# Kernel optimization log

Measured on AMD Instinct MI355X. Metric: run time of the kernel, lower is better.

## Reference

```python
import jax, jax.numpy as jnp
import numpy as np
import math

D = 128
RATIO = 0.8
BN_EPS = 1e-5
N_NODES = 40000
N_EDGES = 640000
Y_SIZE = 8


def _prelu(x, a):
    return jnp.where(x > 0, x, a * x)


def setup_inputs() -> dict:
    key = jax.random.key(0)
    ks = jax.random.split(key, 16)
    inv = lambda n: 1.0 / np.sqrt(n)
    return {
        "x": jax.random.normal(ks[0], (N_NODES, 1), jnp.float32),
        "edge_index": jax.random.randint(ks[1], (2, N_EDGES), 0, N_NODES, jnp.int32),
        "W1": jax.random.normal(ks[2], (1, D), jnp.float32),
        "V1": jax.random.normal(ks[3], (1, D), jnp.float32),
        "Ws": jax.random.normal(ks[4], (9, D, D), jnp.float32) * inv(D),
        "Vs": jax.random.normal(ks[5], (9, D, D), jnp.float32) * inv(D),
        "conv_b": jax.random.normal(ks[6], (10, D), jnp.float32) * 0.01,
        "bn_gamma": 1.0 + 0.1 * jax.random.normal(ks[7], (10, D), jnp.float32),
        "bn_beta": 0.1 * jax.random.normal(ks[8], (10, D), jnp.float32),
        "bn_mean": jnp.zeros((10, D), jnp.float32),
        "bn_var": jnp.ones((10, D), jnp.float32),
        "pool_p": jax.random.normal(ks[9], (10, D), jnp.float32),
        "prelu_a": 0.25 * jnp.ones((1,), jnp.float32),
        "lin1_w": jax.random.normal(ks[10], (2560, 1280), jnp.float32) * inv(2560),
        "lin1_b": jax.random.normal(ks[11], (1280,), jnp.float32) * 0.01,
        "lin2_w": jax.random.normal(ks[12], (1280, Y_SIZE), jnp.float32) * inv(1280),
        "lin2_b": jax.random.normal(ks[13], (Y_SIZE,), jnp.float32) * 0.01,
    }


def reference(x, edge_index, W1, V1, Ws, Vs, conv_b, bn_gamma, bn_beta, bn_mean,
              bn_var, pool_p, prelu_a, lin1_w, lin1_b, lin2_w, lin2_b):
    # Single graph (batch all zeros). Edge array stays fixed size with a validity mask.
    src, dst = edge_index[0], edge_index[1]
    emask = jnp.ones(src.shape, dtype=bool)
    n = x.shape[0]
    h = x
    reads = []
    for i in range(10):
        W = W1 if i == 0 else Ws[i - 1]
        V = V1 if i == 0 else Vs[i - 1]
        # ---- ARMAConv (num_stacks=1, num_layers=1): relu(L_hat (h W) + h V + b)
        ew = emask.astype(h.dtype)
        deg = jax.ops.segment_sum(ew, dst, num_segments=n)
        dinv = jnp.where(deg > 0, 1.0 / jnp.sqrt(deg), 0.0)
        norm = dinv[dst] * dinv[src] * ew                      # [E]
        hw = h @ W                                             # [n, D]
        agg = jax.ops.segment_sum(hw[src] * norm[:, None], dst, num_segments=n)
        h = jax.nn.relu(agg + h @ V + conv_b[i])
        # ---- BatchNorm1d (eval mode, running stats)
        h = (h - bn_mean[i]) * (bn_gamma[i] / jnp.sqrt(bn_var[i] + BN_EPS)) + bn_beta[i]
        # ---- shared PReLU
        h = _prelu(h, prelu_a)
        # ---- TopKPooling(ratio=0.8): score = tanh(h.p/||p||), keep ceil(0.8n)
        p = pool_p[i]
        score = jnp.tanh(h @ p / jnp.linalg.norm(p))
        k = math.ceil(RATIO * n)
        topv, idx = jax.lax.top_k(score, k)
        h = h[idx] * topv[:, None]                             # [k, D]
        remap = jnp.full((n,), -1, jnp.int32).at[idx].set(jnp.arange(k, dtype=jnp.int32))
        ns, nd = remap[src], remap[dst]
        emask = emask & (ns >= 0) & (nd >= 0)
        src = jnp.where(emask, ns, 0)
        dst = jnp.where(emask, nd, 0)
        n = k
        # ---- global max + mean pool (single graph)
        reads.append(jnp.concatenate([h.max(axis=0), h.mean(axis=0)]))
    r = jnp.concatenate(reads)[None, :]                        # [1, 2560]
    z = _prelu(r @ lin1_w + lin1_b, prelu_a)                   # dropout = identity (eval)
    z = _prelu(z @ lin2_w + lin2_b, prelu_a)
    z = z - z.min(axis=1, keepdims=True)
    z = z / z.max(axis=1, keepdims=True)
    z = z / z.sum(axis=1, keepdims=True)
    return z
```

## Files before the change

kernel.cpp:

```cpp
#include <hip/hip_runtime.h>
#include <hip/hip_bf16.h>

#define NEDGE 640000
#define NMAX  40000
#define SB    40
#define PRB   256
#define EBLK  512
#define FB    1280
#define LIN1B 64
#define GRB   8
#define HTS   12
#define TKB   32
#define GHN   5632
#define GBMAX 4096

__device__ inline unsigned orderKey(float s) {
    unsigned b = __float_as_uint(s);
    return (b & 0x80000000u) ? ~b : (b | 0x80000000u);
}

__device__ inline void histAdd(int* sh, int bin, bool act, int nbits) {
    unsigned long long mm = __ballot(act);
    for (int b = 0; b < nbits; b++) {
        unsigned long long bal = __ballot(act && ((bin >> b) & 1));
        mm &= ((bin >> b) & 1) ? bal : ~bal;
    }
    if (act) {
        int lane = threadIdx.x & 63;
        int leader = __ffsll(mm) - 1;
        if (lane == leader) atomicAdd(&sh[bin], __popcll(mm));
    }
}

__device__ inline void gridbar(int* ctr, int target) {
    __syncthreads();
    if (threadIdx.x == 0) {
        __threadfence();
        __hip_atomic_fetch_add(ctr, 1, __ATOMIC_RELEASE, __HIP_MEMORY_SCOPE_AGENT);
        while (__hip_atomic_load(ctr, __ATOMIC_ACQUIRE, __HIP_MEMORY_SCOPE_AGENT) < target)
            __builtin_amdgcn_s_sleep(1);
        __threadfence();
    }
    __syncthreads();
}

__device__ inline int waveScanIncl(int v) {
    int lane = threadIdx.x & 63;
    #pragma unroll
    for (int off = 1; off < 64; off <<= 1) {
        int o = __shfl_up(v, off);
        if (lane >= off) v += o;
    }
    return v;
}

__device__ inline void selScan2048(const int* gh, int rem, int* outD, int* outR, int* outCnt) {
    __shared__ int wtot[16];
    __shared__ int s_T;
    int t = threadIdx.x, lane = t & 63, wid = t >> 6;
    int a0 = gh[2*t], a1 = gh[2*t+1];
    int s  = a0 + a1;
    int ws = waveScanIncl(s);
    if (lane == 63) wtot[wid] = ws;
    __syncthreads();
    if (t < 16) {
        int v = wtot[t];
        #pragma unroll
        for (int off = 1; off < 16; off <<= 1) { int o = __shfl_up(v, off); if (lane >= off) v += o; }
        wtot[t] = v;
        if (t == 15) s_T = v;
    }
    __syncthreads();
    int base = (wid > 0) ? wtot[wid-1] : 0;
    int inclPair = base + ws;
    int P1 = inclPair - a1;
    int P0 = P1 - a0;
    int Q = s_T - rem;
    if (a0 > 0 && P0 <= Q && Q < P0 + a0) { *outD = 2*t;   *outR = a0 - (Q - P0); *outCnt = a0; }
    if (a1 > 0 && P1 <= Q && Q < P1 + a1) { *outD = 2*t+1; *outR = a1 - (Q - P1); *outCnt = a1; }
    __syncthreads();
}

__device__ inline void selScan1024(const int* gh, int rem, int* outD, int* outR, int* outCnt) {
    __shared__ int wtot[16];
    __shared__ int s_T;
    int t = threadIdx.x, lane = t & 63, wid = t >> 6;
    int a0 = gh[t];
    int ws = waveScanIncl(a0);
    if (lane == 63) wtot[wid] = ws;
    __syncthreads();
    if (t < 16) {
        int v = wtot[t];
        #pragma unroll
        for (int off = 1; off < 16; off <<= 1) { int o = __shfl_up(v, off); if (lane >= off) v += o; }
        wtot[t] = v;
        if (t == 15) s_T = v;
    }
    __syncthreads();
    int base = (wid > 0) ? wtot[wid-1] : 0;
    int P0 = base + ws - a0;
    int Q = s_T - rem;
    if (a0 > 0 && P0 <= Q && Q < P0 + a0) { *outD = t; *outR = a0 - (Q - P0); *outCnt = a0; }
    __syncthreads();
}

__device__ inline void prefixSel256(int* lh, const int* gh, int rem, int* outD, int* outR) {
    int t = threadIdx.x;
    if (t < 256) lh[t] = gh[t];
    __syncthreads();
    for (int off = 1; off < 256; off <<= 1) {
        int v = 0;
        if (t < 256) v = lh[t] + ((t >= off) ? lh[t-off] : 0);
        __syncthreads();
        if (t < 256) lh[t] = v;
        __syncthreads();
    }
    if (t < 256) {
        int P = lh[t], Pp = (t == 0) ? 0 : lh[t-1];
        if (P >= rem && Pp < rem) { *outD = t; *outR = rem - Pp; }
    }
    __syncthreads();
}

__device__ inline void poolReduceC(const float* __restrict__ scr, float* __restrict__ rbuf,
                                   int gbP, int L, int ch) {
    int t = threadIdx.x;
    bool isMax = ch < 128;
    float acc = isMax ? -3.402823e38f : 0.f;
    for (int r = t; r < gbP; r += 256) {
        float v = scr[(size_t)r*256 + ch];
        acc = isMax ? fmaxf(acc, v) : (acc + v);
    }
    __shared__ float red[256];
    red[t] = acc; __syncthreads();
    for (int st = 128; st > 0; st >>= 1) {
        if (t < st) red[t] = isMax ? fmaxf(red[t], red[t+st]) : (red[t] + red[t+st]);
        __syncthreads();
    }
    if (t == 0) rbuf[L*256 + ch] = red[0];
}

__device__ const float c_invk[10] = {
    1.0f/32000.0f, 1.0f/25600.0f, 1.0f/20480.0f, 1.0f/16384.0f, 1.0f/13108.0f,
    1.0f/10487.0f, 1.0f/8390.0f,  1.0f/6712.0f,  1.0f/5370.0f,  1.0f/4296.0f };

__global__ void k_init(const int* __restrict__ eidx, int* __restrict__ esrc,
                       int* __restrict__ edst, int* __restrict__ erank,
                       const float* __restrict__ poolp,
                       float* __restrict__ rbuf, float* __restrict__ pnorm,
                       int* __restrict__ ecnt, int* __restrict__ degA,
                       int* __restrict__ tkc) {
    int b = blockIdx.x, t = threadIdx.x;
    if (b < 10) {
        rbuf[b*256 + t] = (t < 128) ? -3.402823e38f : 0.0f;
        __shared__ float red[256];
        float v = 0.0f;
        if (t < 128) { float pv = poolp[b*128 + t]; v = pv*pv; }
        red[t] = v; __syncthreads();
        for (int s = 128; s > 0; s >>= 1) { if (t < s) red[t] += red[t+s]; __syncthreads(); }
        if (t == 0) pnorm[b] = sqrtf(red[0]);
    }
    if (b == 10 && t < 16) ecnt[t] = (t == 0) ? NEDGE : 0;
    if (b == 11 && t < 64) tkc[t] = 0;
    int e = b*256 + t;
    if (e < NEDGE) {
        int d = eidx[NEDGE + e];
        esrc[e] = eidx[e]; edst[e] = d;
        erank[e] = atomicAdd(&degA[d], 1);
    }
}

__global__ __launch_bounds__(256) void k_presum(const int* __restrict__ deg,
                                                int* __restrict__ lbsum,
                                                int n, int chunk) {
    int b = blockIdx.x, t = threadIdx.x;
    __shared__ int red[256];
    int start = b*chunk, end = min(start + chunk, n);
    int s = 0;
    for (int i = start + t; i < end; i += 256) s += deg[i];
    red[t] = s; __syncthreads();
    for (int st = 128; st > 0; st >>= 1) { if (t < st) red[t] += red[t+st]; __syncthreads(); }
    if (t == 0) lbsum[b] = red[0];
}

__global__ void k_scan(const int* __restrict__ deg,
                       int* __restrict__ offs, float* __restrict__ dinv,
                       int* __restrict__ ghist, int* __restrict__ selbuf,
                       const int* __restrict__ lbsum,
                       const float* __restrict__ scr, float* __restrict__ rbuf,
                       int n, int chunk, int gbP, int prevL) {
    int b = blockIdx.x, t = threadIdx.x, lane = t & 63, wid = t >> 6;
    if (b >= SB) {
        if (gbP > 0) poolReduceC(scr, rbuf, gbP, prevL, b - SB);
        return;
    }
    __shared__ int s_excl;
    __shared__ int wsum[4];
    __shared__ int s_carry;
    __shared__ int s_sums[SB];
    if (b == 0) {
        for (int jj = t; jj < GHN; jj += 256) ghist[jj] = 0;
        if (t == 0) { selbuf[2] = 0; selbuf[5] = 0; }
    }
    if (t < SB) s_sums[t] = lbsum[t];
    __syncthreads();
    if (t == 0) {
        int excl = 0;
        for (int p = 0; p < b; p++) excl += s_sums[p];
        s_excl = excl;
    }
    __syncthreads();
    if (t == 0) s_carry = s_excl;
    __syncthreads();
    int start = b*chunk, end = min(start + chunk, n);
    for (int base = start; base < end; base += 256) {
        int i = base + t;
        int d = (i < end) ? deg[i] : 0;
        int incl = d;
        for (int off = 1; off < 64; off <<= 1) {
            int o = __shfl_up(incl, off);
            if (lane >= off) incl += o;
        }
        if (lane == 63) wsum[wid] = incl;
        __syncthreads();
        if (t == 0) { int c = s_carry; for (int w = 0; w < 4; w++) { int tmp = wsum[w]; wsum[w] = c; c += tmp; } s_carry = c; }
        __syncthreads();
        int p = wsum[wid] + incl - d;
        if (i < end) {
            offs[i] = p;
            dinv[i] = (d > 0) ? 1.0f/sqrtf((float)d) : 0.0f;
        }
        __syncthreads();
    }
}

__global__ __launch_bounds__(128) void k_fill(const int* __restrict__ esrc, const int* __restrict__ edst,
                                              const int* __restrict__ erank, const int* __restrict__ offs,
                                              int* __restrict__ csr, const int* __restrict__ ecnt) {
    int ec = *ecnt;
    for (int e = blockIdx.x*128 + threadIdx.x; e < ec; e += FB*128)
        csr[offs[edst[e]] + erank[e]] = esrc[e];
}

__global__ __launch_bounds__(128) void k_gather0(
    const float* __restrict__ x, const float* __restrict__ W1, const float* __restrict__ V1,
    const float* __restrict__ convb,
    const float* __restrict__ bng, const float* __restrict__ bnb,
    const float* __restrict__ bnm, const float* __restrict__ bnv,
    const float* __restrict__ poolp, const float* __restrict__ pnorm,
    const float* __restrict__ prelua,
    const int* __restrict__ offs, const int* __restrict__ deg, const float* __restrict__ dinv,
    const int* __restrict__ csr,
    float* __restrict__ AGG, float* __restrict__ score, unsigned* __restrict__ keys) {
    int v = blockIdx.x, j = threadIdx.x;
    __shared__ float red[128];
    int off = offs[v], dg = deg[v];
    float accs = 0.0f;
    for (int c = j; c < dg; c += 128) { int s = csr[off + c]; accs += x[s]*dinv[s]; }
    red[j] = accs; __syncthreads();
    for (int st = 64; st > 0; st >>= 1) { if (j < st) red[j] += red[j+st]; __syncthreads(); }
    float aggs = red[0] * dinv[v];
    __syncthreads();
    float h2 = aggs*W1[j] + x[v]*V1[j] + convb[j];
    h2 = fmaxf(h2, 0.0f);
    float scale = bng[j] / sqrtf(bnv[j] + 1e-5f);
    h2 = (h2 - bnm[j])*scale + bnb[j];
    float a = prelua[0];
    h2 = (h2 > 0.0f) ? h2 : a*h2;
    AGG[v*128 + j] = h2;
    red[j] = h2 * poolp[j]; __syncthreads();
    for (int st = 64; st > 0; st >>= 1) { if (j < st) red[j] += red[j+st]; __syncthreads(); }
    if (j == 0) {
        float sc = tanhf(red[0] / pnorm[0]);
        score[v] = sc;
        keys[v]  = orderKey(sc);
    }
}

__global__ __launch_bounds__(128) void k_gather(
    const float* __restrict__ HW, float* __restrict__ AGG,
    const int* __restrict__ offs, const int* __restrict__ deg, const float* __restrict__ dinv,
    const int* __restrict__ csr,
    const float* __restrict__ bng, const float* __restrict__ bnb,
    const float* __restrict__ bnm, const float* __restrict__ bnv,
    const float* __restrict__ poolp, const float* __restrict__ pnorm,
    const float* __restrict__ prelua,
    float* __restrict__ score, unsigned* __restrict__ keys, int layer) {
    int v = blockIdx.x, j = threadIdx.x;
    __shared__ int   s_src[128];
    __shared__ float s_dv[128];
    __shared__ float red[128];
    int off = offs[v], dg = deg[v];
    float acc = 0.0f;
    for (int base = 0; base < dg; base += 128) {
        int cnt = min(128, dg - base);
        if (j < cnt) { int s = csr[off + base + j]; s_src[j] = s; s_dv[j] = dinv[s]; }
        __syncthreads();
        for (int c = 0; c < cnt; c++) acc += HW[s_src[c]*128 + j] * s_dv[c];
        __syncthreads();
    }
    int gj = layer*128 + j;
    float h2 = AGG[v*128 + j] + acc*dinv[v];
    h2 = fmaxf(h2, 0.0f);
    float scale = bng[gj] / sqrtf(bnv[gj] + 1e-5f);
    h2 = (h2 - bnm[gj])*scale + bnb[gj];
    float a = prelua[0];
    h2 = (h2 > 0.0f) ? h2 : a*h2;
    AGG[v*128 + j] = h2;
    red[j] = h2 * poolp[gj]; __syncthreads();
    for (int st = 64; st > 0; st >>= 1) { if (j < st) red[j] += red[j+st]; __syncthreads(); }
    if (j == 0) {
        float sc = tanhf(red[0] / pnorm[layer]);
        score[v] = sc;
        keys[v]  = orderKey(sc);
    }
}

__global__ __launch_bounds__(1024) void k_topk(const unsigned* __restrict__ keys,
                                               int* __restrict__ gh, int* __restrict__ selbuf,
                                               int* __restrict__ degN,
                                               int* __restrict__ remap, int* __restrict__ keep_ids,
                                               int* __restrict__ bar, int n, int kk) {
    __shared__ int lh[2048];
    __shared__ int s_d1, s_r1, s_c1, s_dA, s_rA, s_cA, s_dB, s_ntk, s_cnt3, s_bC, s_r2, s_lowD, s_lowR;
    __shared__ int s_base, s_cur;
    int t = threadIdx.x, b = blockIdx.x, lane = t & 63;
    int* h1 = gh;
    int* h2 = gh + 2048;
    int* h3 = gh + 4096;
    int* h4 = gh + 5120;
    int* h5 = gh + 5376;

    for (int i = b*1024 + t; i < NMAX; i += TKB*1024) degN[i] = 0;

    int nR = (n + 1023) & ~1023;
    lh[t] = 0; lh[t+1024] = 0;
    __syncthreads();
    for (int i = b*1024 + t; i < nR; i += TKB*1024) {
        bool act = (i < n);
        int bin = act ? (int)(keys[i] >> 21) : 0;
        histAdd(lh, bin, act, 11);
    }
    __syncthreads();
    { int c = lh[t]; if (c) atomicAdd(&h1[t], c); c = lh[t+1024]; if (c) atomicAdd(&h1[t+1024], c); }
    gridbar(&bar[0], TKB);
    selScan2048(h1, kk, &s_d1, &s_r1, &s_c1);
    int bstar = s_d1;

    lh[t] = 0; lh[t+1024] = 0;
    __syncthreads();
    for (int i = b*1024 + t; i < nR; i += TKB*1024) {
        bool act = false; int bin = 0;
        if (i < n) { unsigned key = keys[i]; act = ((int)(key >> 21) == bstar); bin = (int)((key >> 10) & 2047); }
        histAdd(lh, act ? bin : 0, act, 11);
    }
    __syncthreads();
    { int c = lh[t]; if (c) atomicAdd(&h2[t], c); c = lh[t+1024]; if (c) atomicAdd(&h2[t+1024], c); }
    gridbar(&bar[1], TKB);
    selScan2048(h2, s_r1, &s_dA, &s_rA, &s_cA);
    unsigned top21 = ((unsigned)bstar << 11) | (unsigned)s_dA;

    lh[t] = 0;
    __syncthreads();
    for (int i = b*1024 + t; i < nR; i += TKB*1024) {
        bool act = false; int bin = 0;
        if (i < n) { unsigned key = keys[i]; act = ((key >> 10) == top21); bin = (int)(key & 1023); }
        histAdd(lh, act ? bin : 0, act, 10);
    }
    __syncthreads();
    { int c = lh[t]; if (c) atomicAdd(&h3[t], c); }
    gridbar(&bar[2], TKB);
    selScan1024(h3, s_rA, &s_dB, &s_ntk, &s_cnt3);
    unsigned thresh = (top21 << 10) | (unsigned)s_dB;

    int cut;
    if (s_cnt3 == s_ntk) {
        cut = n - 1;
    } else {
        if (t < 256) lh[t] = 0;
        __syncthreads();
        for (int i = b*1024 + t; i < n; i += TKB*1024)
            if (keys[i] == thresh) atomicAdd(&lh[i >> 8], 1);
        __syncthreads();
        if (t < 256) { int c = lh[t]; if (c) atomicAdd(&h4[t], c); }
        gridbar(&bar[3], TKB);
        prefixSel256(lh, h4, s_ntk, &s_bC, &s_r2);
        int bC = s_bC;

        if (t < 256) lh[t] = 0;
        __syncthreads();
        for (int i = b*1024 + t; i < n; i += TKB*1024)
            if (keys[i] == thresh && (i >> 8) == bC) atomicAdd(&lh[i & 255], 1);
        __syncthreads();
        if (t < 256) { int c = lh[t]; if (c) atomicAdd(&h5[t], c); }
        gridbar(&bar[4], TKB);
        prefixSel256(lh, h5, s_r2, &s_lowD, &s_lowR);
        cut = (bC << 8) | s_lowD;
    }

    {
        int cnt = 0;
        for (int base = b*1024; base < n; base += TKB*1024) {
            int i = base + t;
            if (i < n) {
                unsigned key = keys[i];
                cnt += (key > thresh) || (key == thresh && i <= cut);
            }
        }
        lh[t] = cnt; __syncthreads();
        for (int st = 512; st > 0; st >>= 1) { if (t < st) lh[t] += lh[t+st]; __syncthreads(); }
        if (t == 0) { s_base = atomicAdd(&selbuf[5], lh[0]); s_cur = 0; }
        __syncthreads();
        for (int base = b*1024; base < n; base += TKB*1024) {
            int i = base + t;
            bool keep = false;
            if (i < n) {
                unsigned key = keys[i];
                keep = (key > thresh) || (key == thresh && i <= cut);
            }
            unsigned long long m = __ballot(keep);
            int wcnt = __popcll(m);
            int wbase = 0;
            if (lane == 0 && wcnt) wbase = atomicAdd(&s_cur, wcnt);
            wbase = __shfl(wbase, 0);
            if (keep) {
                int slot = s_base + wbase + __popcll(m & ((1ULL << lane) - 1));
                remap[i] = slot; keep_ids[slot] = i;
            } else if (i < n) remap[i] = -1;
        }
    }
}

__global__ __launch_bounds__(128) void k_poolgemm(
        const float* __restrict__ AGGc, const float* __restrict__ score,
        const int* __restrict__ keep_ids, const int* __restrict__ remap,
        float* __restrict__ scr,
        const int* __restrict__ esrcP, const int* __restrict__ edstP,
        int* __restrict__ esrcN, int* __restrict__ edstN, int* __restrict__ erankN,
        const int* __restrict__ ecntP, int* __restrict__ ecntN, int* __restrict__ degN,
        const float* __restrict__ W, const float* __restrict__ V, const float* __restrict__ bias,
        float* __restrict__ HW, float* __restrict__ AGGn, int k, int gb, int do_gemm) {
    int b = blockIdx.x, t = threadIdx.x;
    __shared__ __align__(16) float ht[128*HTS];
    if (b < gb) {
        int v0 = b * GRB;
        float mx = -3.402823e38f, sm = 0.f;
        #pragma unroll
        for (int it = 0; it < GRB; it++) {
            int r = v0 + it;
            bool valid = (r < k);
            int vv = keep_ids[valid ? r : (k - 1)];
            float val = AGGc[(size_t)vv*128 + t] * score[vv];
            if (!valid) val = 0.f;
            ht[t*HTS + it] = val;
            if (valid) { mx = fmaxf(mx, val); sm += val; }
        }
        scr[b*256 + t]       = mx;
        scr[b*256 + 128 + t] = sm;
        if (!do_gemm) return;
        __syncthreads();
        float accW[GRB], accV[GRB];
        #pragma unroll
        for (int r = 0; r < GRB; r++) { accW[r] = 0.0f; accV[r] = 0.0f; }
        #pragma unroll 4
        for (int kk = 0; kk < 128; kk++) {
            float mw = W[kk*128 + t];
            float mv = V[kk*128 + t];
            const float* hp = &ht[kk*HTS];
            #pragma unroll
            for (int r4 = 0; r4 < GRB; r4 += 4) {
                float4 hq = *(const float4*)(hp + r4);
                accW[r4+0] += hq.x*mw;  accV[r4+0] += hq.x*mv;
                accW[r4+1] += hq.y*mw;  accV[r4+1] += hq.y*mv;
                accW[r4+2] += hq.z*mw;  accV[r4+2] += hq.z*mv;
                accW[r4+3] += hq.w*mw;  accV[r4+3] += hq.w*mv;
            }
        }
        float bb = bias[t];
        #pragma unroll
        for (int r = 0; r < GRB; r++) {
            int v = v0 + r;
            if (v >= k) break;
            HW[(size_t)v*128 + t]   = accW[r];
            AGGn[(size_t)v*128 + t] = accV[r] + bb;
        }
    } else {
        int eb = b - gb, lane = t & 63;
        int ec = *ecntP;
        int* red = (int*)ht;
        __shared__ int s_base, s_cur;
        int cnt = 0;
        for (int base = eb*128; base < ec; base += EBLK*128) {
            int e = base + t;
            if (e < ec) {
                int ns = remap[esrcP[e]], nd = remap[edstP[e]];
                cnt += (ns >= 0 && nd >= 0);
            }
        }
        red[t] = cnt; __syncthreads();
        for (int st = 64; st > 0; st >>= 1) { if (t < st) red[t] += red[t+st]; __syncthreads(); }
        if (t == 0) { s_base = atomicAdd(ecntN, red[0]); s_cur = 0; }
        __syncthreads();
        for (int base = eb*128; base < ec; base += EBLK*128) {
            int e = base + t;
            bool keep = false; int ns = 0, nd = 0;
            if (e < ec) {
                ns = remap[esrcP[e]]; nd = remap[edstP[e]];
                keep = (ns >= 0 && nd >= 0);
            }
            unsigned long long m = __ballot(keep);
            int wcnt = __popcll(m);
            int wbase = 0;
            if (lane == 0 && wcnt) wbase = atomicAdd(&s_cur, wcnt);
            wbase = __shfl(wbase, 0);
            if (keep) {
                int pos = s_base + wbase + __popcll(m & ((1ULL << lane) - 1));
                esrcN[pos] = ns; edstN[pos] = nd;
                erankN[pos] = atomicAdd(&degN[nd], 1);
            }
        }
    }
}

__global__ __launch_bounds__(256) void k_pred(const float* __restrict__ scr, float* __restrict__ rbuf,
                                              int gbP, int L) {
    poolReduceC(scr, rbuf, gbP, L, blockIdx.x);
}

__global__ __launch_bounds__(320) void k_lin1(const float* __restrict__ rbuf,
                                              const float* __restrict__ w1,
                                              float* __restrict__ z1part) {
    int b = blockIdx.x, t = threadIdx.x;
    int j = t*4;
    float4 acc = make_float4(0.f, 0.f, 0.f, 0.f);
    int i0 = b*40;
    for (int r = 0; r < 40; r++) {
        int i = i0 + r;
        float rv = rbuf[i];
        if (i & 128) rv *= c_invk[i >> 8];
        float4 w = *(const float4*)(w1 + (size_t)i*1280 + j);
        acc.x += rv*w.x; acc.y += rv*w.y; acc.z += rv*w.z; acc.w += rv*w.w;
    }
    *(float4*)(z1part + b*1280 + j) = acc;
}

__global__ __launch_bounds__(320) void k_lin2(const float* __restrict__ z1part,
                                              const float* __restrict__ b1,
                                              const float* __restrict__ w2, const float* __restrict__ b2,
                                              const float* __restrict__ prelua, float* __restrict__ out) {
    int t = threadIdx.x, lane = t & 63, wid = t >> 6;
    float a = prelua[0];
    int j = t*4;
    float4 acc = make_float4(0.f, 0.f, 0.f, 0.f);
    for (int p = 0; p < LIN1B; p++) {
        float4 v = *(const float4*)(z1part + p*1280 + j);
        acc.x += v.x; acc.y += v.y; acc.z += v.z; acc.w += v.w;
    }
    float4 bb = *(const float4*)(b1 + j);
    float z0 = acc.x + bb.x; z0 = z0 > 0.f ? z0 : a*z0;
    float z1 = acc.y + bb.y; z1 = z1 > 0.f ? z1 : a*z1;
    float z2 = acc.z + bb.z; z2 = z2 > 0.f ? z2 : a*z2;
    float z3 = acc.w + bb.w; z3 = z3 > 0.f ? z3 : a*z3;
    float s[8];
    #pragma unroll
    for (int o = 0; o < 8; o++)
        s[o] = z0*w2[(j+0)*8+o] + z1*w2[(j+1)*8+o] + z2*w2[(j+2)*8+o] + z3*w2[(j+3)*8+o];
    #pragma unroll
    for (int off = 32; off > 0; off >>= 1)
        #pragma unroll
        for (int o = 0; o < 8; o++) s[o] += __shfl_down(s[o], off);
    __shared__ float sred[5][8];
    if (lane == 0)
        for (int o = 0; o < 8; o++) sred[wid][o] = s[o];
    __syncthreads();
    if (t == 0) {
        float zo[8];
        for (int o = 0; o < 8; o++) {
            float z = sred[0][o]+sred[1][o]+sred[2][o]+sred[3][o]+sred[4][o] + b2[o];
            zo[o] = z > 0.f ? z : a*z;
        }
        float mn = zo[0];
        for (int o = 1; o < 8; o++) mn = fminf(mn, zo[o]);
        float v[8], mx = -3.402823e38f;
        for (int o = 0; o < 8; o++) { v[o] = zo[o] - mn; mx = fmaxf(mx, v[o]); }
        float sm = 0.f;
        for (int o = 0; o < 8; o++) { v[o] = v[o] / mx; sm += v[o]; }
        for (int o = 0; o < 8; o++) out[o] = v[o] / sm;
    }
}

extern "C" void kernel_launch(void* const* d_in, const int* in_sizes, int n_in,
                              void* d_out, int out_size, void* d_ws, size_t ws_size,
                              hipStream_t stream) {
    const float* x      = (const float*)d_in[0];
    const int*   eidx   = (const int*)  d_in[1];
    const float* W1     = (const float*)d_in[2];
    const float* V1     = (const float*)d_in[3];
    const float* Ws     = (const float*)d_in[4];
    const float* Vs     = (const float*)d_in[5];
    const float* convb  = (const float*)d_in[6];
    const float* bng    = (const float*)d_in[7];
    const float* bnb    = (const float*)d_in[8];
    const float* bnm    = (const float*)d_in[9];
    const float* bnv    = (const float*)d_in[10];
    const float* poolp  = (const float*)d_in[11];
    const float* prelua = (const float*)d_in[12];
    const float* w1     = (const float*)d_in[13];
    const float* b1     = (const float*)d_in[14];
    const float* w2     = (const float*)d_in[15];
    const float* b2     = (const float*)d_in[16];
    float* out = (float*)d_out;

    float* wsf  = (float*)d_ws;
    float* aggA   = wsf;
    float* aggB   = aggA  + (size_t)NMAX*128;
    float* HW     = aggB  + (size_t)NMAX*128;
    float* dinv   = HW    + (size_t)NMAX*128;
    float* score  = dinv  + NMAX;
    float* rbuf   = score + NMAX;
    float* pnorm  = rbuf  + 2560;
    float* z1part = pnorm + 16;
    float* scr    = z1part + LIN1B*1280;
    unsigned* keys = (unsigned*)(scr + (size_t)GBMAX*256);
    int* esrcA  = (int*)(keys + NMAX);
    int* edstA  = esrcA + NEDGE;
    int* erankA = edstA + NEDGE;
    int* esrcB  = erankA + NEDGE;
    int* edstB  = esrcB + NEDGE;
    int* erankB = edstB + NEDGE;
    int* csr    = erankB + NEDGE;
    int* degA   = csr   + NEDGE;
    int* degB   = degA  + NMAX;
    int* ghist  = degB  + NMAX;
    int* offs   = ghist + GHN;
    int* remap  = offs  + NMAX;
    int* keep_ids = remap + NMAX;
    int* lbsum  = keep_ids + NMAX;
    int* ecnt   = lbsum + SB*2;
    int* selbuf = ecnt  + 16;
    int* tkc    = selbuf + 16;

    static const int NS[10] = {40000,32000,25600,20480,16384,13108,10487,8390,6712,5370};
    static const int KS[10] = {32000,25600,20480,16384,13108,10487,8390,6712,5370,4296};

    hipMemsetAsync(degA, 0, (size_t)NMAX*sizeof(int), stream);
    k_init<<<2500, 256, 0, stream>>>(eidx, esrcA, edstA, erankA, poolp, rbuf, pnorm,
                                     ecnt, degA, tkc);

    for (int i = 0; i < 10; i++) {
        int n = NS[i], k = KS[i];
        int chunk = (n + SB - 1) / SB;
        int* esrcP  = (i & 1) ? esrcB  : esrcA;
        int* edstP  = (i & 1) ? edstB  : edstA;
        int* erankP = (i & 1) ? erankB : erankA;
        int* esrcN  = (i & 1) ? esrcA  : esrcB;
        int* edstN  = (i & 1) ? edstA  : edstB;
        int* erankN = (i & 1) ? erankA : erankB;
        int* degP   = (i & 1) ? degB : degA;
        int* degN   = (i & 1) ? degA : degB;
        float* AGGc = (i & 1) ? aggB : aggA;
        float* AGGn = (i & 1) ? aggA : aggB;

        int gbP = (i == 0) ? 0 : (KS[i-1] + GRB - 1) / GRB;
        k_presum<<<SB, 256, 0, stream>>>(degP, lbsum, n, chunk);
        k_scan<<<SB + PRB, 256, 0, stream>>>(degP, offs, dinv, ghist, selbuf,
                                             lbsum, scr, rbuf, n, chunk,
                                             gbP, i - 1);

        k_fill<<<FB, 128, 0, stream>>>(esrcP, edstP, erankP, offs, csr, &ecnt[i]);

        if (i == 0) {
            k_gather0<<<n, 128, 0, stream>>>(x, W1, V1, convb,
                                             bng, bnb, bnm, bnv, poolp, pnorm, prelua,
                                             offs, degP, dinv, csr, AGGc, score, keys);
        } else {
            k_gather<<<n, 128, 0, stream>>>(HW, AGGc, offs, degP, dinv, csr,
                                            bng, bnb, bnm, bnv, poolp, pnorm, prelua,
                                            score, keys, i);
        }

        k_topk<<<TKB, 1024, 0, stream>>>(keys, ghist, selbuf, degN,
                                         remap, keep_ids, tkc + i*5, n, k);

        int gb = (k + GRB - 1) / GRB;
        int do_gemm = (i < 9);
        int grid = gb + (do_gemm ? EBLK : 0);
        k_poolgemm<<<grid, 128, 0, stream>>>(AGGc, score, keep_ids, remap, scr,
                                             esrcP, edstP, esrcN, edstN, erankN,
                                             &ecnt[i], &ecnt[i+1], degN,
                                             Ws + (size_t)min(i,8)*16384,
                                             Vs + (size_t)min(i,8)*16384,
                                             convb + min(i+1,9)*128,
                                             HW, AGGn, k, gb, do_gemm);
    }

    k_pred<<<PRB, 256, 0, stream>>>(scr, rbuf, (KS[9] + GRB - 1) / GRB, 9);
    k_lin1<<<LIN1B, 320, 0, stream>>>(rbuf, w1, z1part);
    k_lin2<<<1, 320, 0, stream>>>(z1part, b1, w2, b2, prelua, out);
}
```

Before: 977.9 us.

## Widen poolgemm to 256 threads with split-K, unroll gather, relocate degN clear

k_poolgemm now runs 256-thread blocks whose two halves each cover half of the 128-wide reduction dimension, combining partial sums through shared memory. It is templated on rows per block (16 for the large early layers, 8 later), and its edge-compaction path now handles 256 edges per iteration. The gather loop in k_gather is unrolled by four to keep more independent HW loads in flight. Clearing of degN moves from k_topk to k_presum, and k_topk's grid doubles to 64 blocks. These changes aim for more parallelism and memory-level overlap, at the cost of extra shared-memory reductions and syncs and different per-layer grid sizes.

```diff
diff --git a/kernel.cpp b/kernel.cpp
--- a/kernel.cpp
+++ b/kernel.cpp
@@ -8,9 +8,7 @@
 #define EBLK  512
 #define FB    1280
 #define LIN1B 64
-#define GRB   8
-#define HTS   12
-#define TKB   32
+#define TKB   64
 #define GHN   5632
 #define GBMAX 4096
 
@@ -172,9 +170,11 @@
 
 __global__ __launch_bounds__(256) void k_presum(const int* __restrict__ deg,
                                                 int* __restrict__ lbsum,
+                                                int* __restrict__ degN,
                                                 int n, int chunk) {
     int b = blockIdx.x, t = threadIdx.x;
     __shared__ int red[256];
+    for (int i = b*256 + t; i < NMAX; i += SB*256) degN[i] = 0;
     int start = b*chunk, end = min(start + chunk, n);
     int s = 0;
     for (int i = start + t; i < end; i += 256) s += deg[i];
@@ -296,7 +296,17 @@
         int cnt = min(128, dg - base);
         if (j < cnt) { int s = csr[off + base + j]; s_src[j] = s; s_dv[j] = dinv[s]; }
         __syncthreads();
-        for (int c = 0; c < cnt; c++) acc += HW[s_src[c]*128 + j] * s_dv[c];
+        int c = 0;
+        for (; c + 4 <= cnt; c += 4) {
+            int s0 = s_src[c], s1 = s_src[c+1], s2 = s_src[c+2], s3 = s_src[c+3];
+            float d0 = s_dv[c], d1 = s_dv[c+1], d2 = s_dv[c+2], d3 = s_dv[c+3];
+            float h0 = HW[(size_t)s0*128 + j];
+            float h1 = HW[(size_t)s1*128 + j];
+            float h2 = HW[(size_t)s2*128 + j];
+            float h3 = HW[(size_t)s3*128 + j];
+            acc += h0*d0; acc += h1*d1; acc += h2*d2; acc += h3*d3;
+        }
+        for (; c < cnt; c++) acc += HW[(size_t)s_src[c]*128 + j] * s_dv[c];
         __syncthreads();
     }
     int gj = layer*128 + j;
@@ -318,7 +328,6 @@
 
 __global__ __launch_bounds__(1024) void k_topk(const unsigned* __restrict__ keys,
                                                int* __restrict__ gh, int* __restrict__ selbuf,
-                                               int* __restrict__ degN,
                                                int* __restrict__ remap, int* __restrict__ keep_ids,
                                                int* __restrict__ bar, int n, int kk) {
     __shared__ int lh[2048];
@@ -330,8 +339,6 @@
     int* h3 = gh + 4096;
     int* h4 = gh + 5120;
     int* h5 = gh + 5376;
-
-    for (int i = b*1024 + t; i < NMAX; i += TKB*1024) degN[i] = 0;
 
     int nR = (n + 1023) & ~1023;
     lh[t] = 0; lh[t+1024] = 0;
@@ -431,7 +438,8 @@
     }
 }
 
-__global__ __launch_bounds__(128) void k_poolgemm(
+template<int TGRB>
+__global__ __launch_bounds__(256) void k_poolgemm(
         const float* __restrict__ AGGc, const float* __restrict__ score,
         const int* __restrict__ keep_ids, const int* __restrict__ remap,
         float* __restrict__ scr,
@@ -440,35 +448,44 @@
         const int* __restrict__ ecntP, int* __restrict__ ecntN, int* __restrict__ degN,
         const float* __restrict__ W, const float* __restrict__ V, const float* __restrict__ bias,
         float* __restrict__ HW, float* __restrict__ AGGn, int k, int gb, int do_gemm) {
+    constexpr int THTS = TGRB + 4;
     int b = blockIdx.x, t = threadIdx.x;
-    __shared__ __align__(16) float ht[128*HTS];
+    __shared__ __align__(16) float ht[128*THTS];
+    __shared__ __align__(16) float part[2*TGRB*128];
     if (b < gb) {
-        int v0 = b * GRB;
+        int tt = t & 127, hf = t >> 7;
+        constexpr int RH = TGRB/2;
+        int v0 = b * TGRB;
         float mx = -3.402823e38f, sm = 0.f;
         #pragma unroll
-        for (int it = 0; it < GRB; it++) {
-            int r = v0 + it;
+        for (int it = 0; it < RH; it++) {
+            int r = v0 + hf*RH + it;
             bool valid = (r < k);
             int vv = keep_ids[valid ? r : (k - 1)];
-            float val = AGGc[(size_t)vv*128 + t] * score[vv];
+            float val = AGGc[(size_t)vv*128 + tt] * score[vv];
             if (!valid) val = 0.f;
-            ht[t*HTS + it] = val;
+            ht[tt*THTS + hf*RH + it] = val;
             if (valid) { mx = fmaxf(mx, val); sm += val; }
         }
-        scr[b*256 + t]       = mx;
-        scr[b*256 + 128 + t] = sm;
+        part[hf*128 + tt]       = mx;
+        part[256 + hf*128 + tt] = sm;
+        __syncthreads();
+        if (t < 128) {
+            scr[b*256 + t]       = fmaxf(part[t], part[128 + t]);
+            scr[b*256 + 128 + t] = part[256 + t] + part[384 + t];
+        }
         if (!do_gemm) return;
-        __syncthreads();
-        float accW[GRB], accV[GRB];
+        float accW[TGRB], accV[TGRB];
         #pragma unroll
-        for (int r = 0; r < GRB; r++) { accW[r] = 0.0f; accV[r] = 0.0f; }
+        for (int r = 0; r < TGRB; r++) { accW[r] = 0.0f; accV[r] = 0.0f; }
+        int kk0 = hf * 64, kk1 = kk0 + 64;
         #pragma unroll 4
-        for (int kk = 0; kk < 128; kk++) {
-            float mw = W[kk*128 + t];
-            float mv = V[kk*128 + t];
-            const float* hp = &ht[kk*HTS];
+        for (int kk = kk0; kk < kk1; kk++) {
+            float mw = W[kk*128 + tt];
+            float mv = V[kk*128 + tt];
+            const float* hp = &ht[kk*THTS];
             #pragma unroll
-            for (int r4 = 0; r4 < GRB; r4 += 4) {
+            for (int r4 = 0; r4 < TGRB; r4 += 4) {
                 float4 hq = *(const float4*)(hp + r4);
                 accW[r4+0] += hq.x*mw;  accV[r4+0] += hq.x*mv;
                 accW[r4+1] += hq.y*mw;  accV[r4+1] += hq.y*mv;
@@ -476,13 +493,26 @@
                 accW[r4+3] += hq.w*mw;  accV[r4+3] += hq.w*mv;
             }
         }
-        float bb = bias[t];
-        #pragma unroll
-        for (int r = 0; r < GRB; r++) {
-            int v = v0 + r;
-            if (v >= k) break;
-            HW[(size_t)v*128 + t]   = accW[r];
-            AGGn[(size_t)v*128 + t] = accV[r] + bb;
+        __syncthreads();
+        if (hf == 1) {
+            #pragma unroll
+            for (int r = 0; r < TGRB; r++) {
+                part[(2*r+0)*128 + tt] = accW[r];
+                part[(2*r+1)*128 + tt] = accV[r];
+            }
+        }
+        __syncthreads();
+        if (hf == 0) {
+            float bb = bias[tt];
+            #pragma unroll
+            for (int r = 0; r < TGRB; r++) {
+                int v = v0 + r;
+                if (v >= k) break;
+                float w2 = accW[r] + part[(2*r+0)*128 + tt];
+                float v2 = accV[r] + part[(2*r+1)*128 + tt];
+                HW[(size_t)v*128 + tt]   = w2;
+                AGGn[(size_t)v*128 + tt] = v2 + bb;
+            }
         }
     } else {
         int eb = b - gb, lane = t & 63;
@@ -490,7 +520,7 @@
         int* red = (int*)ht;
         __shared__ int s_base, s_cur;
         int cnt = 0;
-        for (int base = eb*128; base < ec; base += EBLK*128) {
+        for (int base = eb*256; base < ec; base += EBLK*256) {
             int e = base + t;
             if (e < ec) {
                 int ns = remap[esrcP[e]], nd = remap[edstP[e]];
@@ -498,10 +528,10 @@
             }
         }
         red[t] = cnt; __syncthreads();
-        for (int st = 64; st > 0; st >>= 1) { if (t < st) red[t] += red[t+st]; __syncthreads(); }
+        for (int st = 128; st > 0; st >>= 1) { if (t < st) red[t] += red[t+st]; __syncthreads(); }
         if (t == 0) { s_base = atomicAdd(ecntN, red[0]); s_cur = 0; }
         __syncthreads();
-        for (int base = eb*128; base < ec; base += EBLK*128) {
+        for (int base = eb*256; base < ec; base += EBLK*256) {
             int e = base + t;
             bool keep = false; int ns = 0, nd = 0;
             if (e < ec) {
@@ -642,6 +672,10 @@
 
     static const int NS[10] = {40000,32000,25600,20480,16384,13108,10487,8390,6712,5370};
     static const int KS[10] = {32000,25600,20480,16384,13108,10487,8390,6712,5370,4296};
+    static const int GRBS[10] = {16,16,16,16,8,8,8,8,8,8};
+
+    int gbs[10];
+    for (int i = 0; i < 10; i++) gbs[i] = (KS[i] + GRBS[i] - 1) / GRBS[i];
 
     hipMemsetAsync(degA, 0, (size_t)NMAX*sizeof(int), stream);
     k_init<<<2500, 256, 0, stream>>>(eidx, esrcA, edstA, erankA, poolp, rbuf, pnorm,
@@ -661,8 +695,8 @@
         float* AGGc = (i & 1) ? aggB : aggA;
         float* AGGn = (i & 1) ? aggA : aggB;
 
-        int gbP = (i == 0) ? 0 : (KS[i-1] + GRB - 1) / GRB;
-        k_presum<<<SB, 256, 0, stream>>>(degP, lbsum, n, chunk);
+        int gbP = (i == 0) ? 0 : gbs[i-1];
+        k_presum<<<SB, 256, 0, stream>>>(degP, lbsum, degN, n, chunk);
         k_scan<<<SB + PRB, 256, 0, stream>>>(degP, offs, dinv, ghist, selbuf,
                                              lbsum, scr, rbuf, n, chunk,
                                              gbP, i - 1);
@@ -679,22 +713,32 @@
                                             score, keys, i);
         }
 
-        k_topk<<<TKB, 1024, 0, stream>>>(keys, ghist, selbuf, degN,
+        k_topk<<<TKB, 1024, 0, stream>>>(keys, ghist, selbuf,
                                          remap, keep_ids, tkc + i*5, n, k);
 
-        int gb = (k + GRB - 1) / GRB;
+        int gb = gbs[i];
         int do_gemm = (i < 9);
         int grid = gb + (do_gemm ? EBLK : 0);
-        k_poolgemm<<<grid, 128, 0, stream>>>(AGGc, score, keep_ids, remap, scr,
-                                             esrcP, edstP, esrcN, edstN, erankN,
-                                             &ecnt[i], &ecnt[i+1], degN,
-                                             Ws + (size_t)min(i,8)*16384,
-                                             Vs + (size_t)min(i,8)*16384,
-                                             convb + min(i+1,9)*128,
-                                             HW, AGGn, k, gb, do_gemm);
-    }
-
-    k_pred<<<PRB, 256, 0, stream>>>(scr, rbuf, (KS[9] + GRB - 1) / GRB, 9);
+        if (GRBS[i] == 16) {
+            k_poolgemm<16><<<grid, 256, 0, stream>>>(AGGc, score, keep_ids, remap, scr,
+                                                     esrcP, edstP, esrcN, edstN, erankN,
+                                                     &ecnt[i], &ecnt[i+1], degN,
+                                                     Ws + (size_t)min(i,8)*16384,
+                                                     Vs + (size_t)min(i,8)*16384,
+                                                     convb + min(i+1,9)*128,
+                                                     HW, AGGn, k, gb, do_gemm);
+        } else {
+            k_poolgemm<8><<<grid, 256, 0, stream>>>(AGGc, score, keep_ids, remap, scr,
+                                                    esrcP, edstP, esrcN, edstN, erankN,
+                                                    &ecnt[i], &ecnt[i+1], degN,
+                                                    Ws + (size_t)min(i,8)*16384,
+                                                    Vs + (size_t)min(i,8)*16384,
+                                                    convb + min(i+1,9)*128,
+                                                    HW, AGGn, k, gb, do_gemm);
+        }
+    }
+
+    k_pred<<<PRB, 256, 0, stream>>>(scr, rbuf, gbs[9], 9);
     k_lin1<<<LIN1B, 320, 0, stream>>>(rbuf, w1, z1part);
     k_lin2<<<1, 320, 0, stream>>>(z1part, b1, w2, b2, prelua, out);
 }
```

Result: no change. 975.5 us (-0.2%).
